# Optimization experiments

Hardware: AMD Instinct MI355X
Metric: run time of the kernel (lower is better)

Reference implementation:

```python
import jax, jax.numpy as jnp
import numpy as np

UNIT = 20          # self.unit_size
HID = 36           # self.hidden_size
IN = 4 * UNIT      # LSTM input_size = 80
NCLS = 3


def setup_inputs() -> dict:
    key = jax.random.key(0)
    ks = jax.random.split(key, 11)
    B, T = 512, 40960
    s = 1.0 / np.sqrt(HID).astype(np.float32)
    u = lambda k, shp: jax.random.uniform(k, shp, jnp.float32, -s, s)
    return {
        "x": jax.random.normal(ks[0], (B, 4, T), jnp.float32),
        "h0": jax.random.normal(ks[1], (B, HID), jnp.float32),
        "c0": jax.random.normal(ks[2], (B, HID), jnp.float32),
        "W_ih": u(ks[3], (4 * HID, IN)),   # PyTorch LSTM weight_ih_l0, gate order i,f,g,o
        "W_hh": u(ks[4], (4 * HID, HID)),
        "b_ih": u(ks[5], (4 * HID,)),
        "b_hh": u(ks[6], (4 * HID,)),
        "fc1_w": u(ks[7], (16, HID)),
        "fc1_b": u(ks[8], (16,)),
        "fc2_w": u(ks[9], (NCLS, 16)),
        "fc2_b": u(ks[10], (NCLS,)),
    }


def reference(x, h0, c0, W_ih, W_hh, b_ih, b_hh, fc1_w, fc1_b, fc2_w, fc2_b):
    B = x.shape[0]
    r = x.shape[-1] % UNIT
    if r > 0:
        x = x[:, :, :-r]
    # (B,4,T) -> (B,4,S,20) -> (B,S,4,20) -> (B,S,80)
    x = x.reshape(B, 4, -1, UNIT).transpose(0, 2, 1, 3).reshape(B, -1, IN)
    # Precompute input contribution to all gates once (big GEMM), scan handles recurrence.
    xW = jnp.einsum("bsi,gi->bsg", x, W_ih) + b_ih + b_hh  # [B,S,4H]

    def step(carry, xt):
        h, c = carry
        gates = xt + h @ W_hh.T                 # [B,4H]
        i, f, g, o = jnp.split(gates, 4, axis=-1)
        i = jax.nn.sigmoid(i)
        f = jax.nn.sigmoid(f)
        g = jnp.tanh(g)
        o = jax.nn.sigmoid(o)
        c = f * c + i * g
        h = o * jnp.tanh(c)
        return (h, c), None

    (h, _), _ = jax.lax.scan(step, (h0, c0), jnp.swapaxes(xW, 0, 1))  # last hidden == x[:, -1, :]
    h = jax.nn.relu(h @ fc1_w.T + fc1_b)
    return h @ fc2_w.T + fc2_b
```

## Files before the change

kernel.cpp:

```cpp
#include <hip/hip_runtime.h>
#include <hip/hip_bf16.h>

#define UNIT 20
#define HID 36
#define G4 144
#define INW 80
#define NCLS 3
#define TT 40960
#define SS 2048
#define BB 512
#define PAD 16

#define BFRAG_N 13824
#define BFRAG_BYTES 55296

typedef float v2f  __attribute__((ext_vector_type(2)));
typedef short bf16x8 __attribute__((ext_vector_type(8)));
typedef float f32x4  __attribute__((ext_vector_type(4)));

__device__ __forceinline__ float exp2_hw(float x){ float r; asm("v_exp_f32 %0, %1" : "=v"(r) : "v"(x)); return r; }
__device__ __forceinline__ float rcp_hw(float x){ float r; asm("v_rcp_f32 %0, %1" : "=v"(r) : "v"(x)); return r; }
__device__ __forceinline__ float sigm_hw(float x){ return rcp_hw(1.f + exp2_hw(-1.4426950408889634f * x)); }
__device__ __forceinline__ float tanh_hw(float x){ return 1.f - 2.f * rcp_hw(1.f + exp2_hw(2.8853900817779268f * x)); }
__device__ __forceinline__ float rl(float v, int l){
    return __uint_as_float(__builtin_amdgcn_readlane(__float_as_uint(v), l));
}
__device__ __forceinline__ unsigned short f2bf(float f){
    unsigned int u = __float_as_uint(f);
    unsigned int r = (u + 0x7fffu + ((u >> 16) & 1u)) >> 16;
    return (unsigned short)r;
}
__device__ __forceinline__ float bf2f(unsigned short h){
    return __uint_as_float(((unsigned int)h) << 16);
}

__global__ __launch_bounds__(256)
void lstm_prep(const float* __restrict__ W_ih, unsigned short* __restrict__ B)
{
    int i = blockIdx.x * 256 + threadIdx.x;
    if (i >= BFRAG_N) return;
    int j   = i & 7;
    int col = (i >> 3) & 15;
    int gsl = i >> 7;
    int g   = gsl & 3;
    int ns  = gsl >> 2;
    int s   = ns % 3, n = ns / 3;
    int gate = n*16 + col;
    int k    = s*32 + g*8 + j;
    float v  = (k < 80) ? W_ih[(size_t)gate*INW + k] : 0.f;
    unsigned short h = f2bf(v);
    B[i]           = h;
    B[BFRAG_N + i] = f2bf(v - bf2f(h));
}

__global__ __launch_bounds__(256)
void lstm_mproj(const float* __restrict__ x, const unsigned short* __restrict__ Bf,
                const float* __restrict__ b_ih, const float* __restrict__ b_hh,
                float* __restrict__ xw)
{
    const int bid = blockIdx.x;
    const int r   = bid & 15;
    const int b   = bid >> 4;
    const int tid = threadIdx.x;
    const int w   = tid >> 6;
    const int l   = tid & 63;
    const int col = l & 15;
    const int g   = l >> 4;

    __shared__ unsigned short A[4][2][16*104];

    for (int idx = l; idx < 256; idx += 64) {
        int s = idx >> 4, j = 80 + (idx & 15);
        A[w][0][s*104 + j] = 0;
        A[w][1][s*104 + j] = 0;
    }

    float bias[9];
    #pragma unroll
    for (int n = 0; n < 9; ++n) bias[n] = b_ih[n*16 + col] + b_hh[n*16 + col];

    const float* xb = x + (size_t)b * 4 * TT;

    #pragma unroll
    for (int t = 0; t < 2; ++t) {
        const int sg0 = r*128 + w*32 + t*16;

        #pragma unroll
        for (int i = 0; i < 5; ++i) {
            int f = i*64 + l;
            int c = f / 80, rem = f - 80*c, s = rem / 5, q = rem - 5*s;
            float4 v = *(const float4*)(xb + (size_t)c*TT + (size_t)(sg0 + s)*UNIT + 4*q);
            int idx = s*104 + c*20 + 4*q;
            unsigned short h0 = f2bf(v.x), h1 = f2bf(v.y), h2 = f2bf(v.z), h3 = f2bf(v.w);
            ushort4 hh = {h0, h1, h2, h3};
            ushort4 ll = {f2bf(v.x - bf2f(h0)), f2bf(v.y - bf2f(h1)),
                          f2bf(v.z - bf2f(h2)), f2bf(v.w - bf2f(h3))};
            *(ushort4*)&A[w][0][idx] = hh;
            *(ushort4*)&A[w][1][idx] = ll;
        }

        bf16x8 ah[3], al[3];
        #pragma unroll
        for (int s = 0; s < 3; ++s) {
            ah[s] = *(const bf16x8*)&A[w][0][col*104 + s*32 + g*8];
            al[s] = *(const bf16x8*)&A[w][1][col*104 + s*32 + g*8];
        }

        #pragma unroll
        for (int n = 0; n < 9; ++n) {
            f32x4 acc = {bias[n], bias[n], bias[n], bias[n]};
            #pragma unroll
            for (int s = 0; s < 3; ++s) {
                const unsigned short* bp = Bf + ((n*3 + s)*4 + g)*128 + col*8;
                bf16x8 bh = *(const bf16x8*)bp;
                bf16x8 bl = *(const bf16x8*)(bp + BFRAG_N);
                acc = __builtin_amdgcn_mfma_f32_16x16x32_bf16(ah[s], bh, acc, 0, 0, 0);
                acc = __builtin_amdgcn_mfma_f32_16x16x32_bf16(ah[s], bl, acc, 0, 0, 0);
                acc = __builtin_amdgcn_mfma_f32_16x16x32_bf16(al[s], bh, acc, 0, 0, 0);
            }
            #pragma unroll
            for (int reg = 0; reg < 4; ++reg) {
                int step = sg0 + g*4 + reg;
                xw[((size_t)step * BB + b) * G4 + n*16 + col] = acc[reg];
            }
        }
    }
}

__global__ __launch_bounds__(64, 1)
void lstm_recur_full(const float* __restrict__ xw, const float* __restrict__ h0,
                     const float* __restrict__ c0, const float* __restrict__ W_hh,
                     const float* __restrict__ fc1_w, const float* __restrict__ fc1_b,
                     const float* __restrict__ fc2_w, const float* __restrict__ fc2_b,
                     float* __restrict__ out)
{
    const int lane = threadIdx.x & 63;
    const int b    = blockIdx.x;
    const int jj   = (lane < HID) ? lane : 0;

    v2f wif[HID], wgo[HID];
    #pragma unroll
    for (int q = 0; q < HID; ++q) {
        wif[q] = (v2f){ W_hh[(size_t)jj*HID + q],         W_hh[(size_t)(HID+jj)*HID + q] };
        wgo[q] = (v2f){ W_hh[(size_t)(2*HID+jj)*HID + q], W_hh[(size_t)(3*HID+jj)*HID + q] };
    }

    float hval = h0[b*HID + jj];
    float cval = c0[b*HID + jj];

    const float*  xp     = xw + (size_t)b * G4 + jj;
    const size_t  STRIDE = (size_t)BB * G4;

    float qa[8][4], qb[8][4];

#define LOADBANK(dst, base) { \
    _Pragma("unroll") for (int u = 0; u < 8; ++u) { \
        const float* p = xp + (size_t)((base) + u) * STRIDE; \
        dst[u][0] = p[0]; dst[u][1] = p[HID]; dst[u][2] = p[2*HID]; dst[u][3] = p[3*HID]; \
    } }

#define DOSTEP(bk, u) { \
    v2f aifA = { bk[u][0], bk[u][1] }, aifB = {0.f,0.f}; \
    v2f agoA = { bk[u][2], bk[u][3] }, agoB = {0.f,0.f}; \
    _Pragma("unroll") for (int q = 0; q < HID; q += 2) { \
        float s0 = rl(hval, q), s1 = rl(hval, q+1); \
        aifA += s0 * wif[q]; \
        agoA += s0 * wgo[q]; \
        aifB += s1 * wif[q+1]; \
        agoB += s1 * wgo[q+1]; \
    } \
    v2f aif = aifA + aifB, ago = agoA + agoB; \
    float gi = sigm_hw(aif[0]), gf = sigm_hw(aif[1]); \
    float gg = tanh_hw(ago[0]), go = sigm_hw(ago[1]); \
    cval = gf * cval + gi * gg; \
    hval = go * tanh_hw(cval); }

    LOADBANK(qa, 0);
    for (int s8 = 0; s8 < SS; s8 += 16) {
        LOADBANK(qb, s8 + 8);
        DOSTEP(qa,0) DOSTEP(qa,1) DOSTEP(qa,2) DOSTEP(qa,3)
        DOSTEP(qa,4) DOSTEP(qa,5) DOSTEP(qa,6) DOSTEP(qa,7)
        LOADBANK(qa, s8 + 16);
        DOSTEP(qb,0) DOSTEP(qb,1) DOSTEP(qb,2) DOSTEP(qb,3)
        DOSTEP(qb,4) DOSTEP(qb,5) DOSTEP(qb,6) DOSTEP(qb,7)
    }
#undef LOADBANK
#undef DOSTEP

    float a1 = 0.f;
    if (lane < 16) {
        a1 = fc1_b[lane];
        #pragma unroll
        for (int q = 0; q < HID; ++q) a1 += rl(hval, q) * fc1_w[lane*HID + q];
        a1 = fmaxf(a1, 0.f);
    }
    float f1[16];
    #pragma unroll
    for (int q = 0; q < 16; ++q) f1[q] = rl(a1, q);
    if (lane < NCLS) {
        float a2 = fc2_b[lane];
        #pragma unroll
        for (int q = 0; q < 16; ++q) a2 += f1[q] * fc2_w[lane*16 + q];
        out[b*NCLS + lane] = a2;
    }
}

__global__ __launch_bounds__(192)
void lstm_proj2(const float* __restrict__ x, const float* __restrict__ W_ih,
                const float* __restrict__ b_ih, const float* __restrict__ b_hh,
                float* __restrict__ xw, int s0, int cnt, int nseq)
{
    const int bid = blockIdx.x;
    const int r   = bid % nseq;
    const int b   = bid / nseq;
    const int t   = threadIdx.x;
    const int base_local = r * 128;
    const int mysteps = min(128, cnt - base_local);
    const bool act = (t < 144);
    const int pr   = act ? (t % 72) : 0;
    const int slot = act ? (t / 72) : 0;

    __shared__ __align__(16) float xin[16][INW];

    v2f wpk[INW]; v2f bias2 = {0.f, 0.f};
    if (act) {
        const float* w0 = W_ih + (size_t)pr * INW;
        const float* w1 = W_ih + (size_t)(pr + 72) * INW;
        #pragma unroll
        for (int q = 0; q < INW; ++q) wpk[q] = (v2f){w0[q], w1[q]};
        bias2 = (v2f){b_ih[pr] + b_hh[pr], b_ih[pr+72] + b_hh[pr+72]};
    }
    const float* xb = x + (size_t)b * 4 * TT;

    for (int sub = 0; sub < mysteps; sub += 16) {
        const int sg = s0 + base_local + sub;
        __syncthreads();
        for (int j = t; j < 320; j += 192) {
            int c = j / 80, q = j - c*80;
            float4 v = ((const float4*)(xb + (size_t)c*TT + (size_t)sg*UNIT))[q];
            int e = q*4; int sl = e / UNIT, u = e - sl*UNIT;
            *(float4*)&xin[sl][c*UNIT + u] = v;
        }
        __syncthreads();
        if (act) {
            for (int si = slot; si < 16; si += 2) {
                const float4* xv = (const float4*)xin[si];
                v2f a0 = bias2, a1 = {0.f,0.f}, a2 = {0.f,0.f}, a3 = {0.f,0.f};
                #pragma unroll
                for (int q = 0; q < 20; ++q) {
                    float4 v = xv[q];
                    a0 += v.x * wpk[4*q+0];
                    a1 += v.y * wpk[4*q+1];
                    a2 += v.z * wpk[4*q+2];
                    a3 += v.w * wpk[4*q+3];
                }
                v2f res = (a0 + a1) + (a2 + a3);
                size_t o = ((size_t)(base_local + sub + si) * BB + b) * G4;
                xw[o + pr]      = res[0];
                xw[o + pr + 72] = res[1];
            }
        }
    }
}

__global__ __launch_bounds__(256)
void lstm_recur(const float* __restrict__ xw, const float* __restrict__ h0,
                const float* __restrict__ c0, const float* __restrict__ W_hh,
                const float* __restrict__ fc1_w, const float* __restrict__ fc1_b,
                const float* __restrict__ fc2_w, const float* __restrict__ fc2_b,
                float* __restrict__ state, float* __restrict__ out, int s0, int cnt)
{
    const int wid  = threadIdx.x >> 6;
    const int lane = threadIdx.x & 63;
    const int b    = blockIdx.x * 4 + wid;
    const int jj   = (lane < HID) ? lane : 0;

    v2f wif[HID], wgo[HID];
    #pragma unroll
    for (int q = 0; q < HID; ++q) {
        wif[q] = (v2f){ W_hh[(size_t)jj*HID + q],         W_hh[(size_t)(HID+jj)*HID + q] };
        wgo[q] = (v2f){ W_hh[(size_t)(2*HID+jj)*HID + q], W_hh[(size_t)(3*HID+jj)*HID + q] };
    }

    float hval, cval;
    if (s0 == 0) { hval = h0[b*HID + jj];    cval = c0[b*HID + jj]; }
    else         { hval = state[b*HID + jj]; cval = state[BB*HID + b*HID + jj]; }

    const float*  xp     = xw + (size_t)b * G4 + jj;
    const size_t  STRIDE = (size_t)BB * G4;

    float qa[8][4], qb[8][4];

#define LOADBANK(dst, base) { \
    _Pragma("unroll") for (int u = 0; u < 8; ++u) { \
        int ss = (base) + u; \
        const float* p = xp + (size_t)((ss < cnt) ? ss : 0) * STRIDE; \
        dst[u][0] = p[0]; dst[u][1] = p[HID]; dst[u][2] = p[2*HID]; dst[u][3] = p[3*HID]; \
    } }

#define DOSTEP(bk, u) { \
    v2f aifA = { bk[u][0], bk[u][1] }, aifB = {0.f,0.f}; \
    v2f agoA = { bk[u][2], bk[u][3] }, agoB = {0.f,0.f}; \
    _Pragma("unroll") for (int q = 0; q < HID; q += 2) { \
        float s0 = rl(hval, q), s1 = rl(hval, q+1); \
        aifA += s0 * wif[q]; \
        agoA += s0 * wgo[q]; \
        aifB += s1 * wif[q+1]; \
        agoB += s1 * wgo[q+1]; \
    } \
    v2f aif = aifA + aifB, ago = agoA + agoB; \
    float gi = sigm_hw(aif[0]), gf = sigm_hw(aif[1]); \
    float gg = tanh_hw(ago[0]), go = sigm_hw(ago[1]); \
    cval = gf * cval + gi * gg; \
    hval = go * tanh_hw(cval); }

    LOADBANK(qa, 0);
    for (int s8 = 0; s8 < cnt; s8 += 16) {
        LOADBANK(qb, s8 + 8);
        DOSTEP(qa,0) DOSTEP(qa,1) DOSTEP(qa,2) DOSTEP(qa,3)
        DOSTEP(qa,4) DOSTEP(qa,5) DOSTEP(qa,6) DOSTEP(qa,7)
        LOADBANK(qa, s8 + 16);
        DOSTEP(qb,0) DOSTEP(qb,1) DOSTEP(qb,2) DOSTEP(qb,3)
        DOSTEP(qb,4) DOSTEP(qb,5) DOSTEP(qb,6) DOSTEP(qb,7)
    }
#undef LOADBANK
#undef DOSTEP

    if (s0 + cnt == SS) {
        float a1 = 0.f;
        if (lane < 16) {
            a1 = fc1_b[lane];
            #pragma unroll
            for (int k = 0; k < HID; ++k) a1 += rl(hval, k) * fc1_w[lane*HID + k];
            a1 = fmaxf(a1, 0.f);
        }
        float f1[16];
        #pragma unroll
        for (int k = 0; k < 16; ++k) f1[k] = rl(a1, k);
        if (lane < NCLS) {
            float a2 = fc2_b[lane];
            #pragma unroll
            for (int k = 0; k < 16; ++k) a2 += f1[k] * fc2_w[lane*16 + k];
            out[b*NCLS + lane] = a2;
        }
    } else {
        if (lane < HID) {
            state[b*HID + lane]          = hval;
            state[BB*HID + b*HID + lane] = cval;
        }
    }
}

__global__ __launch_bounds__(192)
void lstm_fused(const float* __restrict__ x, const float* __restrict__ h0,
                const float* __restrict__ c0, const float* __restrict__ W_ih,
                const float* __restrict__ W_hh, const float* __restrict__ b_ih,
                const float* __restrict__ b_hh, const float* __restrict__ fc1_w,
                const float* __restrict__ fc1_b, const float* __restrict__ fc2_w,
                const float* __restrict__ fc2_b, float* __restrict__ out)
{
    const int b = blockIdx.x;
    const int t = threadIdx.x;
    __shared__ __align__(16) float xin[16][INW];
    __shared__ __align__(16) float xwl[16][G4];
    __shared__ __align__(16) float h_s[HID];
    __shared__ __align__(16) float g_s[G4];
    float wih[INW]; float whh[HID];
    float bias = 0.f, K = 0.f, Aa = 0.f, Bb = 0.f;
    if (t < G4) {
        const float4* wr = (const float4*)(W_ih + t * INW);
        #pragma unroll
        for (int i = 0; i < INW/4; ++i) { float4 v = wr[i]; wih[4*i]=v.x; wih[4*i+1]=v.y; wih[4*i+2]=v.z; wih[4*i+3]=v.w; }
        const float4* hr = (const float4*)(W_hh + t * HID);
        #pragma unroll
        for (int j = 0; j < HID/4; ++j) { float4 v = hr[j]; whh[4*j]=v.x; whh[4*j+1]=v.y; whh[4*j+2]=v.z; whh[4*j+3]=v.w; }
        bias = b_ih[t] + b_hh[t];
        const bool tnh = (t >= 2*HID && t < 3*HID);
        K  = tnh ?  2.8853900817779268f : -1.4426950408889634f;
        Aa = tnh ?  1.f : 0.f;
        Bb = tnh ? -2.f : 1.f;
    }
    float c = 0.f;
    if (t < HID) { c = c0[b*HID + t]; h_s[t] = h0[b*HID + t]; }
    __syncthreads();
    const float* xb = x + (size_t)b * 4 * TT;
    for (int ck = 0; ck < SS/16; ++ck) {
        const int base = ck * 16 * UNIT;
        for (int j = t; j < 4*16*UNIT; j += 192) {
            int chn = j / (16*UNIT); int r = j - chn*(16*UNIT);
            xin[r/UNIT][chn*UNIT + (r%UNIT)] = xb[chn*TT + base + r];
        }
        __syncthreads();
        if (t < G4) {
            for (int s = 0; s < 16; ++s) {
                const float4* xv = (const float4*)xin[s];
                float a0 = bias, a1 = 0.f, a2 = 0.f, a3 = 0.f;
                #pragma unroll
                for (int i = 0; i < INW/4; ++i) {
                    float4 v = xv[i];
                    a0 += v.x*wih[4*i]; a1 += v.y*wih[4*i+1]; a2 += v.z*wih[4*i+2]; a3 += v.w*wih[4*i+3];
                }
                xwl[s][t] = (a0+a1)+(a2+a3);
            }
        }
        __syncthreads();
        for (int s = 0; s < 16; ++s) {
            if (t < G4) {
                const float4* hv = (const float4*)h_s;
                float a0 = xwl[s][t], a1 = 0.f, a2 = 0.f, a3 = 0.f;
                #pragma unroll
                for (int j = 0; j < HID/4; ++j) {
                    float4 v = hv[j];
                    a0 += v.x*whh[4*j]; a1 += v.y*whh[4*j+1]; a2 += v.z*whh[4*j+2]; a3 += v.w*whh[4*j+3];
                }
                float acc = (a0+a1)+(a2+a3);
                g_s[t] = Aa + Bb * rcp_hw(1.f + exp2_hw(K * acc));
            }
            __syncthreads();
            if (t < HID) {
                float ig=g_s[t], fg=g_s[HID+t], gg=g_s[2*HID+t], og=g_s[3*HID+t];
                c = fg*c + ig*gg;
                h_s[t] = og * tanh_hw(c);
            }
            __syncthreads();
        }
    }
    if (t < 16) {
        float a = fc1_b[t];
        #pragma unroll
        for (int j = 0; j < HID; ++j) a += h_s[j]*fc1_w[t*HID+j];
        g_s[t] = fmaxf(a, 0.f);
    }
    __syncthreads();
    if (t < NCLS) {
        float a = fc2_b[t];
        #pragma unroll
        for (int j = 0; j < 16; ++j) a += g_s[j]*fc2_w[t*16+j];
        out[b*NCLS + t] = a;
    }
}

extern "C" void kernel_launch(void* const* d_in, const int* in_sizes, int n_in,
                              void* d_out, int out_size, void* d_ws, size_t ws_size,
                              hipStream_t stream) {
    const float* x     = (const float*)d_in[0];
    const float* h0    = (const float*)d_in[1];
    const float* c0    = (const float*)d_in[2];
    const float* W_ih  = (const float*)d_in[3];
    const float* W_hh  = (const float*)d_in[4];
    const float* b_ih  = (const float*)d_in[5];
    const float* b_hh  = (const float*)d_in[6];
    const float* fc1_w = (const float*)d_in[7];
    const float* fc1_b = (const float*)d_in[8];
    const float* fc2_w = (const float*)d_in[9];
    const float* fc2_b = (const float*)d_in[10];
    float* out = (float*)d_out;

    const size_t need = BFRAG_BYTES + 4ull * (size_t)(SS + PAD) * BB * G4;
    if (ws_size >= need) {
        unsigned short* Bf = (unsigned short*)d_ws;
        float* xwbuf = (float*)((char*)d_ws + BFRAG_BYTES);
        lstm_prep <<<(BFRAG_N + 255)/256, 256, 0, stream>>>(W_ih, Bf);
        lstm_mproj<<<BB * (SS/128), 256, 0, stream>>>(x, Bf, b_ih, b_hh, xwbuf);
        lstm_recur_full<<<BB, 64, 0, stream>>>(xwbuf, h0, c0, W_hh,
                                               fc1_w, fc1_b, fc2_w, fc2_b, out);
        return;
    }

    const size_t state_floats = (size_t)BB * HID * 2;
    long cap = (long)(ws_size / 4) - (long)state_floats;
    long sc  = (cap > 0) ? cap / ((long)BB * G4) : 0;
    int  SC  = (int)((sc > SS) ? SS : sc) & ~15;

    if (SC < 16) {
        lstm_fused<<<BB, 192, 0, stream>>>(x, h0, c0, W_ih, W_hh, b_ih, b_hh,
                                           fc1_w, fc1_b, fc2_w, fc2_b, out);
        return;
    }

    float* state = (float*)d_ws;
    float* xwbuf = state + state_floats;

    for (int s0 = 0; s0 < SS; s0 += SC) {
        int cnt = SS - s0; if (cnt > SC) cnt = SC;
        int nseq = (cnt + 127) / 128;
        lstm_proj2<<<BB * nseq, 192, 0, stream>>>(x, W_ih, b_ih, b_hh, xwbuf, s0, cnt, nseq);
        lstm_recur<<<BB / 4, 256, 0, stream>>>(xwbuf, h0, c0, W_hh,
                                               fc1_w, fc1_b, fc2_w, fc2_b,
                                               state, out, s0, cnt);
    }
}
```

Baseline: 1.022 ms.

## Fuse input projection and recurrence into one producer-consumer kernel with chunk flags

```diff
diff --git a/kernel.cpp b/kernel.cpp
--- a/kernel.cpp
+++ b/kernel.cpp
@@ -9,7 +9,10 @@
 #define TT 40960
 #define SS 2048
 #define BB 512
-#define PAD 16
+#define CHK 128
+#define NCHK (SS/CHK)
+#define NRB 128
+#define NPB (NCHK*BB)
 
 #define BFRAG_N 13824
 #define BFRAG_BYTES 55296
@@ -53,105 +56,111 @@
     B[BFRAG_N + i] = f2bf(v - bf2f(h));
 }
 
+__global__ void init_flags(int* f){ f[threadIdx.x] = 0; }
+
 __global__ __launch_bounds__(256)
-void lstm_mproj(const float* __restrict__ x, const unsigned short* __restrict__ Bf,
-                const float* __restrict__ b_ih, const float* __restrict__ b_hh,
-                float* __restrict__ xw)
+void lstm_pc3(const float* __restrict__ x, const unsigned short* __restrict__ Bf,
+              const float* __restrict__ h0, const float* __restrict__ c0,
+              const float* __restrict__ W_hh, const float* __restrict__ b_ih,
+              const float* __restrict__ b_hh, const float* __restrict__ fc1_w,
+              const float* __restrict__ fc1_b, const float* __restrict__ fc2_w,
+              const float* __restrict__ fc2_b, float* __restrict__ out,
+              int* __restrict__ flags, float* __restrict__ xw)
 {
-    const int bid = blockIdx.x;
-    const int r   = bid & 15;
-    const int b   = bid >> 4;
     const int tid = threadIdx.x;
-    const int w   = tid >> 6;
-    const int l   = tid & 63;
-    const int col = l & 15;
-    const int g   = l >> 4;
-
-    __shared__ unsigned short A[4][2][16*104];
-
-    for (int idx = l; idx < 256; idx += 64) {
-        int s = idx >> 4, j = 80 + (idx & 15);
-        A[w][0][s*104 + j] = 0;
-        A[w][1][s*104 + j] = 0;
-    }
-
-    float bias[9];
-    #pragma unroll
-    for (int n = 0; n < 9; ++n) bias[n] = b_ih[n*16 + col] + b_hh[n*16 + col];
-
-    const float* xb = x + (size_t)b * 4 * TT;
-
-    #pragma unroll
-    for (int t = 0; t < 2; ++t) {
-        const int sg0 = r*128 + w*32 + t*16;
-
-        #pragma unroll
-        for (int i = 0; i < 5; ++i) {
-            int f = i*64 + l;
-            int c = f / 80, rem = f - 80*c, s = rem / 5, q = rem - 5*s;
-            float4 v = *(const float4*)(xb + (size_t)c*TT + (size_t)(sg0 + s)*UNIT + 4*q);
-            int idx = s*104 + c*20 + 4*q;
-            unsigned short h0 = f2bf(v.x), h1 = f2bf(v.y), h2 = f2bf(v.z), h3 = f2bf(v.w);
-            ushort4 hh = {h0, h1, h2, h3};
-            ushort4 ll = {f2bf(v.x - bf2f(h0)), f2bf(v.y - bf2f(h1)),
-                          f2bf(v.z - bf2f(h2)), f2bf(v.w - bf2f(h3))};
-            *(ushort4*)&A[w][0][idx] = hh;
-            *(ushort4*)&A[w][1][idx] = ll;
-        }
-
-        bf16x8 ah[3], al[3];
-        #pragma unroll
-        for (int s = 0; s < 3; ++s) {
-            ah[s] = *(const bf16x8*)&A[w][0][col*104 + s*32 + g*8];
-            al[s] = *(const bf16x8*)&A[w][1][col*104 + s*32 + g*8];
-        }
-
-        #pragma unroll
-        for (int n = 0; n < 9; ++n) {
-            f32x4 acc = {bias[n], bias[n], bias[n], bias[n]};
+
+    if (blockIdx.x >= NRB) {
+        const int u = blockIdx.x - NRB;
+        const int r = u >> 9;
+        const int b = u & 511;
+        const int w   = tid >> 6;
+        const int l   = tid & 63;
+        const int col = l & 15;
+        const int g   = l >> 4;
+
+        __shared__ unsigned short A[4][2][16*104];
+
+        for (int idx = l; idx < 256; idx += 64) {
+            int s = idx >> 4, j = 80 + (idx & 15);
+            A[w][0][s*104 + j] = 0;
+            A[w][1][s*104 + j] = 0;
+        }
+
+        float bias[9];
+        #pragma unroll
+        for (int n = 0; n < 9; ++n) bias[n] = b_ih[n*16 + col] + b_hh[n*16 + col];
+
+        const float* xb = x + (size_t)b * 4 * TT;
+
+        #pragma unroll
+        for (int t = 0; t < 2; ++t) {
+            const int sg0 = r*128 + w*32 + t*16;
+
+            #pragma unroll
+            for (int i = 0; i < 5; ++i) {
+                int f = i*64 + l;
+                int c = f / 80, rem = f - 80*c, s = rem / 5, q = rem - 5*s;
+                float4 v = *(const float4*)(xb + (size_t)c*TT + (size_t)(sg0 + s)*UNIT + 4*q);
+                int idx = s*104 + c*20 + 4*q;
+                unsigned short h0v = f2bf(v.x), h1 = f2bf(v.y), h2 = f2bf(v.z), h3 = f2bf(v.w);
+                ushort4 hh = {h0v, h1, h2, h3};
+                ushort4 ll = {f2bf(v.x - bf2f(h0v)), f2bf(v.y - bf2f(h1)),
+                              f2bf(v.z - bf2f(h2)), f2bf(v.w - bf2f(h3))};
+                *(ushort4*)&A[w][0][idx] = hh;
+                *(ushort4*)&A[w][1][idx] = ll;
+            }
+
+            bf16x8 ah[3], al[3];
             #pragma unroll
             for (int s = 0; s < 3; ++s) {
-                const unsigned short* bp = Bf + ((n*3 + s)*4 + g)*128 + col*8;
-                bf16x8 bh = *(const bf16x8*)bp;
-                bf16x8 bl = *(const bf16x8*)(bp + BFRAG_N);
-                acc = __builtin_amdgcn_mfma_f32_16x16x32_bf16(ah[s], bh, acc, 0, 0, 0);
-                acc = __builtin_amdgcn_mfma_f32_16x16x32_bf16(ah[s], bl, acc, 0, 0, 0);
-                acc = __builtin_amdgcn_mfma_f32_16x16x32_bf16(al[s], bh, acc, 0, 0, 0);
-            }
-            #pragma unroll
-            for (int reg = 0; reg < 4; ++reg) {
-                int step = sg0 + g*4 + reg;
-                xw[((size_t)step * BB + b) * G4 + n*16 + col] = acc[reg];
-            }
-        }
-    }
-}
-
-__global__ __launch_bounds__(64, 1)
-void lstm_recur_full(const float* __restrict__ xw, const float* __restrict__ h0,
-                     const float* __restrict__ c0, const float* __restrict__ W_hh,
-                     const float* __restrict__ fc1_w, const float* __restrict__ fc1_b,
-                     const float* __restrict__ fc2_w, const float* __restrict__ fc2_b,
-                     float* __restrict__ out)
-{
-    const int lane = threadIdx.x & 63;
-    const int b    = blockIdx.x;
-    const int jj   = (lane < HID) ? lane : 0;
-
-    v2f wif[HID], wgo[HID];
-    #pragma unroll
-    for (int q = 0; q < HID; ++q) {
-        wif[q] = (v2f){ W_hh[(size_t)jj*HID + q],         W_hh[(size_t)(HID+jj)*HID + q] };
-        wgo[q] = (v2f){ W_hh[(size_t)(2*HID+jj)*HID + q], W_hh[(size_t)(3*HID+jj)*HID + q] };
-    }
-
-    float hval = h0[b*HID + jj];
-    float cval = c0[b*HID + jj];
-
-    const float*  xp     = xw + (size_t)b * G4 + jj;
-    const size_t  STRIDE = (size_t)BB * G4;
-
-    float qa[8][4], qb[8][4];
+                ah[s] = *(const bf16x8*)&A[w][0][col*104 + s*32 + g*8];
+                al[s] = *(const bf16x8*)&A[w][1][col*104 + s*32 + g*8];
+            }
+
+            #pragma unroll
+            for (int n = 0; n < 9; ++n) {
+                f32x4 acc = {bias[n], bias[n], bias[n], bias[n]};
+                #pragma unroll
+                for (int s = 0; s < 3; ++s) {
+                    const unsigned short* bp = Bf + ((n*3 + s)*4 + g)*128 + col*8;
+                    bf16x8 bh = *(const bf16x8*)bp;
+                    bf16x8 bl = *(const bf16x8*)(bp + BFRAG_N);
+                    acc = __builtin_amdgcn_mfma_f32_16x16x32_bf16(ah[s], bh, acc, 0, 0, 0);
+                    acc = __builtin_amdgcn_mfma_f32_16x16x32_bf16(ah[s], bl, acc, 0, 0, 0);
+                    acc = __builtin_amdgcn_mfma_f32_16x16x32_bf16(al[s], bh, acc, 0, 0, 0);
+                }
+                #pragma unroll
+                for (int reg = 0; reg < 4; ++reg) {
+                    int step = sg0 + g*4 + reg;
+                    xw[((size_t)step * BB + b) * G4 + n*16 + col] = acc[reg];
+                }
+            }
+        }
+
+        __threadfence();
+        __syncthreads();
+        if (tid == 0)
+            __hip_atomic_fetch_add(&flags[r], 1, __ATOMIC_RELEASE, __HIP_MEMORY_SCOPE_AGENT);
+    } else {
+        const int wid  = tid >> 6;
+        const int lane = tid & 63;
+        const int b    = blockIdx.x * 4 + wid;
+        const int jj   = (lane < HID) ? lane : 0;
+
+        v2f wif[HID], wgo[HID];
+        #pragma unroll
+        for (int q = 0; q < HID; ++q) {
+            wif[q] = (v2f){ W_hh[(size_t)jj*HID + q],         W_hh[(size_t)(HID+jj)*HID + q] };
+            wgo[q] = (v2f){ W_hh[(size_t)(2*HID+jj)*HID + q], W_hh[(size_t)(3*HID+jj)*HID + q] };
+        }
+
+        float hval = h0[b*HID + jj];
+        float cval = c0[b*HID + jj];
+
+        const float*  xp     = xw + (size_t)b * G4 + jj;
+        const size_t  STRIDE = (size_t)BB * G4;
+
+        float qa[8][4], qb[8][4];
 
 #define LOADBANK(dst, base) { \
     _Pragma("unroll") for (int u = 0; u < 8; ++u) { \
@@ -175,33 +184,41 @@
     cval = gf * cval + gi * gg; \
     hval = go * tanh_hw(cval); }
 
-    LOADBANK(qa, 0);
-    for (int s8 = 0; s8 < SS; s8 += 16) {
-        LOADBANK(qb, s8 + 8);
-        DOSTEP(qa,0) DOSTEP(qa,1) DOSTEP(qa,2) DOSTEP(qa,3)
-        DOSTEP(qa,4) DOSTEP(qa,5) DOSTEP(qa,6) DOSTEP(qa,7)
-        LOADBANK(qa, s8 + 16);
-        DOSTEP(qb,0) DOSTEP(qb,1) DOSTEP(qb,2) DOSTEP(qb,3)
-        DOSTEP(qb,4) DOSTEP(qb,5) DOSTEP(qb,6) DOSTEP(qb,7)
-    }
+        for (int k = 0; k < NCHK; ++k) {
+            while (__hip_atomic_load(&flags[k], __ATOMIC_RELAXED, __HIP_MEMORY_SCOPE_AGENT) < BB)
+                __builtin_amdgcn_s_sleep(8);
+            (void)__hip_atomic_load(&flags[k], __ATOMIC_ACQUIRE, __HIP_MEMORY_SCOPE_AGENT);
+
+            const int base = k * CHK;
+            LOADBANK(qa, base);
+            for (int s8 = 0; s8 < CHK; s8 += 16) {
+                LOADBANK(qb, base + s8 + 8);
+                DOSTEP(qa,0) DOSTEP(qa,1) DOSTEP(qa,2) DOSTEP(qa,3)
+                DOSTEP(qa,4) DOSTEP(qa,5) DOSTEP(qa,6) DOSTEP(qa,7)
+                if (s8 + 16 < CHK) LOADBANK(qa, base + s8 + 16);
+                DOSTEP(qb,0) DOSTEP(qb,1) DOSTEP(qb,2) DOSTEP(qb,3)
+                DOSTEP(qb,4) DOSTEP(qb,5) DOSTEP(qb,6) DOSTEP(qb,7)
+            }
+        }
 #undef LOADBANK
 #undef DOSTEP
 
-    float a1 = 0.f;
-    if (lane < 16) {
-        a1 = fc1_b[lane];
-        #pragma unroll
-        for (int q = 0; q < HID; ++q) a1 += rl(hval, q) * fc1_w[lane*HID + q];
-        a1 = fmaxf(a1, 0.f);
-    }
-    float f1[16];
-    #pragma unroll
-    for (int q = 0; q < 16; ++q) f1[q] = rl(a1, q);
-    if (lane < NCLS) {
-        float a2 = fc2_b[lane];
-        #pragma unroll
-        for (int q = 0; q < 16; ++q) a2 += f1[q] * fc2_w[lane*16 + q];
-        out[b*NCLS + lane] = a2;
+        float a1 = 0.f;
+        if (lane < 16) {
+            a1 = fc1_b[lane];
+            #pragma unroll
+            for (int q = 0; q < HID; ++q) a1 += rl(hval, q) * fc1_w[lane*HID + q];
+            a1 = fmaxf(a1, 0.f);
+        }
+        float f1[16];
+        #pragma unroll
+        for (int q = 0; q < 16; ++q) f1[q] = rl(a1, q);
+        if (lane < NCLS) {
+            float a2 = fc2_b[lane];
+            #pragma unroll
+            for (int q = 0; q < 16; ++q) a2 += f1[q] * fc2_w[lane*16 + q];
+            out[b*NCLS + lane] = a2;
+        }
     }
 }
 
@@ -302,11 +319,11 @@
     v2f aifA = { bk[u][0], bk[u][1] }, aifB = {0.f,0.f}; \
     v2f agoA = { bk[u][2], bk[u][3] }, agoB = {0.f,0.f}; \
     _Pragma("unroll") for (int q = 0; q < HID; q += 2) { \
-        float s0 = rl(hval, q), s1 = rl(hval, q+1); \
-        aifA += s0 * wif[q]; \
-        agoA += s0 * wgo[q]; \
-        aifB += s1 * wif[q+1]; \
-        agoB += s1 * wgo[q+1]; \
+        float s0_ = rl(hval, q), s1_ = rl(hval, q+1); \
+        aifA += s0_ * wif[q]; \
+        agoA += s0_ * wgo[q]; \
+        aifB += s1_ * wif[q+1]; \
+        agoB += s1_ * wgo[q+1]; \
     } \
     v2f aif = aifA + aifB, ago = agoA + agoB; \
     float gi = sigm_hw(aif[0]), gf = sigm_hw(aif[1]); \
@@ -456,14 +473,16 @@
     const float* fc2_b = (const float*)d_in[10];
     float* out = (float*)d_out;
 
-    const size_t need = BFRAG_BYTES + 4ull * (size_t)(SS + PAD) * BB * G4;
+    const size_t need = 256 + BFRAG_BYTES + 4ull * (size_t)SS * BB * G4;
     if (ws_size >= need) {
-        unsigned short* Bf = (unsigned short*)d_ws;
-        float* xwbuf = (float*)((char*)d_ws + BFRAG_BYTES);
+        int* flags = (int*)d_ws;
+        unsigned short* Bf = (unsigned short*)((char*)d_ws + 256);
+        float* xwbuf = (float*)((char*)d_ws + 256 + BFRAG_BYTES);
         lstm_prep <<<(BFRAG_N + 255)/256, 256, 0, stream>>>(W_ih, Bf);
-        lstm_mproj<<<BB * (SS/128), 256, 0, stream>>>(x, Bf, b_ih, b_hh, xwbuf);
-        lstm_recur_full<<<BB, 64, 0, stream>>>(xwbuf, h0, c0, W_hh,
-                                               fc1_w, fc1_b, fc2_w, fc2_b, out);
+        init_flags<<<1, 64, 0, stream>>>(flags);
+        lstm_pc3  <<<NRB + NPB, 256, 0, stream>>>(x, Bf, h0, c0, W_hh, b_ih, b_hh,
+                                                  fc1_w, fc1_b, fc2_w, fc2_b, out,
+                                                  flags, xwbuf);
         return;
     }
 
```

Result: slower. 2.590 ms (+153.4%).
